# Optimization experiments

Hardware: AMD Instinct MI355X
Metric: run time of the kernel (lower is better)

Reference implementation:

```python
import jax, jax.numpy as jnp
import numpy as np

B, C_HIGH, C_LOW, H, W = 4, 256, 128, 64, 64
HEADS = 4
HEAD_DIM = C_LOW // HEADS
FFN = 2 * C_LOW
EPS = 1e-5


def group_norm1(x, w, b):
    # GroupNorm(num_groups=1): normalize over (C,H,W) per sample, per-channel affine
    mu = jnp.mean(x, axis=(1, 2, 3), keepdims=True)
    var = jnp.var(x, axis=(1, 2, 3), keepdims=True)
    xn = (x - mu) * jax.lax.rsqrt(var + EPS)
    return xn * w[None, :, None, None] + b[None, :, None, None]


def conv1x1(x, Wm):
    # 1x1 conv, no bias: Wm [C_out, C_in], x [B,C_in,H,W]
    return jnp.einsum('oc,bchw->bohw', Wm, x)


def setup_inputs() -> dict:
    key = jax.random.key(0)
    ks = jax.random.split(key, 10)
    s = 0.05
    return {
        'high_feature': jax.random.normal(ks[0], (B, C_HIGH, H, W), jnp.float32),
        'low_feature': jax.random.normal(ks[1], (B, C_LOW, H, W), jnp.float32),
        'norm_high_w': jnp.ones((C_HIGH,), jnp.float32),
        'norm_high_b': jnp.zeros((C_HIGH,), jnp.float32),
        'norm_low_w': jnp.ones((C_LOW,), jnp.float32),
        'norm_low_b': jnp.zeros((C_LOW,), jnp.float32),
        'norm_ffn_w': jnp.ones((C_LOW,), jnp.float32),
        'norm_ffn_b': jnp.zeros((C_LOW,), jnp.float32),
        'Wq': jax.random.normal(ks[2], (C_LOW, C_HIGH), jnp.float32) * s,
        'Wk': jax.random.normal(ks[3], (C_LOW, C_LOW), jnp.float32) * s,
        'Wv': jax.random.normal(ks[4], (C_LOW, C_LOW), jnp.float32) * s,
        'Wproj': jax.random.normal(ks[5], (C_LOW, C_LOW), jnp.float32) * s,
        'Wffn1': jax.random.normal(ks[6], (FFN, C_LOW), jnp.float32) * s,
        'Wffn2': jax.random.normal(ks[7], (C_LOW, FFN), jnp.float32) * s,
        # nn.Parameter(torch.zeros(1)) in the original; use 0.1 for nontrivial grads
        'gamma_attn': jnp.full((1,), 0.1, jnp.float32),
        'gamma_ffn': jnp.full((1,), 0.1, jnp.float32),
    }


def reference(high_feature, low_feature, norm_high_w, norm_high_b, norm_low_w,
              norm_low_b, norm_ffn_w, norm_ffn_b, Wq, Wk, Wv, Wproj, Wffn1,
              Wffn2, gamma_attn, gamma_ffn):
    Bb, _, Hh, Ww = low_feature.shape
    N = Hh * Ww
    scale = HEAD_DIM ** (-0.5)

    high_norm = group_norm1(high_feature, norm_high_w, norm_high_b)
    low_norm = group_norm1(low_feature, norm_low_w, norm_low_b)

    q = conv1x1(high_norm, Wq).reshape(Bb, HEADS, HEAD_DIM, N).transpose(0, 1, 3, 2)  # [B,h,N,d]
    k = conv1x1(low_norm, Wk).reshape(Bb, HEADS, HEAD_DIM, N)                         # [B,h,d,N]
    v = conv1x1(low_norm, Wv).reshape(Bb, HEADS, HEAD_DIM, N).transpose(0, 1, 3, 2)   # [B,h,N,d]

    attn = jax.nn.softmax(jnp.einsum('bhnd,bhdm->bhnm', q, k) * scale, axis=-1)       # [B,h,N,N]
    out = jnp.einsum('bhnm,bhmd->bhnd', attn, v)                                      # [B,h,N,d]
    out = out.transpose(0, 1, 3, 2).reshape(Bb, C_LOW, Hh, Ww)
    out = conv1x1(out, Wproj)

    x = low_feature + gamma_attn[0] * out
    xn = group_norm1(x, norm_ffn_w, norm_ffn_b)
    ffn = conv1x1(jax.nn.gelu(conv1x1(xn, Wffn1), approximate=False), Wffn2)
    return x + gamma_ffn[0] * ffn
```

## Files before the change

### kernel.cpp

```cpp
#include <hip/hip_runtime.h>
#include <hip/hip_bf16.h>
#include <math.h>

#define EPS 1e-5f
#define BB 4
#define CHIGH 256
#define CLOW 128
#define NN 4096
#define NHEADS 4
#define HDIM 32
#define FFN_DIM 256
#define SPLITS 4

typedef __bf16 b8 __attribute__((ext_vector_type(8)));
typedef float f4 __attribute__((ext_vector_type(4)));

__device__ __forceinline__ unsigned int cvt_pk(float lo, float hi) {
    float2 t; t.x = lo; t.y = hi;
    __hip_bfloat162 h = __float22bfloat162_rn(t);
    unsigned int r;
    __builtin_memcpy(&r, &h, sizeof(r));
    return r;
}
__device__ __forceinline__ float b2f(unsigned short u) {
    unsigned int x = ((unsigned int)u) << 16;
    float f;
    __builtin_memcpy(&f, &x, 4);
    return f;
}
__device__ __forceinline__ float fexp2(float x) {
#if __has_builtin(__builtin_amdgcn_exp2f)
    return __builtin_amdgcn_exp2f(x);
#else
    return exp2f(x);
#endif
}

__global__ __launch_bounds__(256)
void prep_kernel(const float* __restrict__ high, const float* __restrict__ low,
                 float* __restrict__ acc,
                 const float* __restrict__ w0, const float* __restrict__ w1,
                 const float* __restrict__ w2, const float* __restrict__ w3,
                 const float* __restrict__ w4, const float* __restrict__ w5,
                 unsigned short* __restrict__ dst)
{
    const int z = blockIdx.z;
    if (z < 2) {
        const int perSample = z == 0 ? CHIGH * NN : CLOW * NN;
        const float* X = z == 0 ? high : low;
        float* ac = acc + (z == 0 ? 0 : 8);
        const int b = blockIdx.y;
        const float4* xp = (const float4*)(X + (size_t)b * perSample);
        const int n4 = perSample >> 2;
        const int stride = gridDim.x * blockDim.x;
        int i = blockIdx.x * blockDim.x + threadIdx.x;
        float s = 0.f, s2 = 0.f, sB = 0.f, s2B = 0.f;
        for (; i + stride < n4; i += 2 * stride) {
            float4 v = xp[i];
            float4 u = xp[i + stride];
            s  += v.x + v.y + v.z + v.w;
            s2 += v.x * v.x + v.y * v.y + v.z * v.z + v.w * v.w;
            sB  += u.x + u.y + u.z + u.w;
            s2B += u.x * u.x + u.y * u.y + u.z * u.z + u.w * u.w;
        }
        if (i < n4) {
            float4 v = xp[i];
            s  += v.x + v.y + v.z + v.w;
            s2 += v.x * v.x + v.y * v.y + v.z * v.z + v.w * v.w;
        }
        s += sB; s2 += s2B;
        for (int off = 32; off; off >>= 1) {
            s  += __shfl_down(s, off, 64);
            s2 += __shfl_down(s2, off, 64);
        }
        __shared__ float ls[4], ls2[4];
        const int w = threadIdx.x >> 6;
        if ((threadIdx.x & 63) == 0) { ls[w] = s; ls2[w] = s2; }
        __syncthreads();
        if (threadIdx.x == 0) {
            atomicAdd(&ac[2 * b], ls[0] + ls[1] + ls[2] + ls[3]);
            atomicAdd(&ac[2 * b + 1], ls2[0] + ls2[1] + ls2[2] + ls2[3]);
        }
    } else {
        const int idx = blockIdx.y * 64 + blockIdx.x;
        const int m = idx >> 5;
        if (m >= 6) return;
        const int sizes[6] = {32768, 16384, 16384, 16384, 32768, 32768};
        const int offs[6]  = {0, 32768, 49152, 65536, 81920, 114688};
        const int Ks[6]    = {256, 128, 128, 128, 128, 256};
        const float* src = m == 0 ? w0 : m == 1 ? w1 : m == 2 ? w2 : m == 3 ? w3
                         : m == 4 ? w4 : w5;
        const int i = ((idx & 31) * 256 + threadIdx.x) * 4;
        if (i >= sizes[m]) return;
        const int K = Ks[m];
        const int row = i / K, col = i % K;
        const int mt = row >> 4, mr = row & 15;
        const int kt = col >> 5, kr = col & 31;
        float4 v = *(const float4*)&src[i];
        uint2 pk;
        pk.x = cvt_pk(v.x, v.y);
        pk.y = cvt_pk(v.z, v.w);
        const int doff = offs[m] + (((mt * (K >> 5)) + kt) << 9) + (mr << 5) + kr;
        *(uint2*)&dst[doff] = pk;
    }
}

__global__ __launch_bounds__(256)
void qkv_kernel(const unsigned short* __restrict__ wbf,
                const float* __restrict__ high, const float* __restrict__ low,
                unsigned short* __restrict__ Qt, unsigned short* __restrict__ Kt,
                unsigned short* __restrict__ Vt,
                const float* __restrict__ nh_w, const float* __restrict__ nh_b,
                const float* __restrict__ nl_w, const float* __restrict__ nl_b,
                const float* __restrict__ st)
{
    __shared__ unsigned short XsRaw[32 * 264];
    const int b = blockIdx.y;
    const int n0 = blockIdx.x * 32;
    const int t = threadIdx.x;
    const int w = t >> 6, lm = t & 15, quad = (t & 63) >> 4;
    const int fo = lm * 32 + quad * 8;
    unsigned int* xw = (unsigned int*)XsRaw;

    if (blockIdx.z == 0) {
        const float invCnt = 1.0f / ((float)CHIGH * NN);
        const float mean = st[2 * b] * invCnt;
        const float rstd = rsqrtf(st[2 * b + 1] * invCnt - mean * mean + EPS);
        const float* Xb = high + (size_t)b * CHIGH * NN;
        float4 ra[4], rb[4];
        float wa[4], wb_[4], ca[4], cb[4];
        #pragma unroll
        for (int it = 0; it < 4; it++) {
            const int s = it * 256 + t;
            const int kp = s >> 3;
            const int k2 = kp << 1;
            const int nc = (s & 7) << 2;
            const size_t ro = (size_t)k2 * NN + n0 + nc;
            ra[it] = *(const float4*)&Xb[ro];
            rb[it] = *(const float4*)&Xb[ro + NN];
            wa[it] = nh_w[k2]; wb_[it] = nh_w[k2 + 1];
            ca[it] = nh_b[k2]; cb[it] = nh_b[k2 + 1];
        }
        #pragma unroll
        for (int it = 0; it < 4; it++) {
            const int s = it * 256 + t;
            const int kp = s >> 3;
            const int nc = (s & 7) << 2;
            float4 pa = ra[it], pb = rb[it];
            const float sc0 = wa[it] * rstd,  sb0 = ca[it] - mean * sc0;
            const float sc1 = wb_[it] * rstd, sb1 = cb[it] - mean * sc1;
            pa.x = pa.x * sc0 + sb0; pa.y = pa.y * sc0 + sb0;
            pa.z = pa.z * sc0 + sb0; pa.w = pa.w * sc0 + sb0;
            pb.x = pb.x * sc1 + sb1; pb.y = pb.y * sc1 + sb1;
            pb.z = pb.z * sc1 + sb1; pb.w = pb.w * sc1 + sb1;
            xw[(nc + 0) * 132 + kp] = cvt_pk(pa.x, pb.x);
            xw[(nc + 1) * 132 + kp] = cvt_pk(pa.y, pb.y);
            xw[(nc + 2) * 132 + kp] = cvt_pk(pa.z, pb.z);
            xw[(nc + 3) * 132 + kp] = cvt_pk(pa.w, pb.w);
        }
        __syncthreads();
        const int ng = w & 1, mh = w >> 1;
        f4 acc[4];
        #pragma unroll
        for (int f = 0; f < 4; f++) acc[f] = (f4){0.f, 0.f, 0.f, 0.f};
        #pragma unroll
        for (int kc = 0; kc < 8; kc++) {
            b8 bx = *(const b8*)&XsRaw[(ng * 16 + lm) * 264 + kc * 32 + quad * 8];
            #pragma unroll
            for (int f = 0; f < 4; f++) {
                b8 af = *(const b8*)&wbf[(((mh * 4 + f) * 8 + kc) << 9) + fo];
                acc[f] = __builtin_amdgcn_mfma_f32_16x16x32_bf16(af, bx, acc[f], 0, 0, 0);
            }
        }
        const int n = n0 + ng * 16 + lm;
        const float oscale = 0.25503480f;
        #pragma unroll
        for (int f = 0; f < 4; f++) {
            const int mb = mh * 64 + f * 16 + quad * 4;
            const int hh = mb >> 5, ddb = mb & 31;
            uint2 pk;
            pk.x = cvt_pk(acc[f][0] * oscale, acc[f][1] * oscale);
            pk.y = cvt_pk(acc[f][2] * oscale, acc[f][3] * oscale);
            *(uint2*)&Qt[((size_t)(b * NHEADS + hh) * NN + n) * 32 + ddb] = pk;
        }
    } else {
        const unsigned short* Wb = wbf + 32768;
        const float invCnt = 1.0f / ((float)CLOW * NN);
        const float mean = st[8 + 2 * b] * invCnt;
        const float rstd = rsqrtf(st[8 + 2 * b + 1] * invCnt - mean * mean + EPS);
        const float* Xb = low + (size_t)b * CLOW * NN;
        float4 ra[2], rb[2];
        float wa[2], wb_[2], ca[2], cb[2];
        #pragma unroll
        for (int it = 0; it < 2; it++) {
            const int s = it * 256 + t;
            const int kp = s >> 3;
            const int k2 = kp << 1;
            const int nc = (s & 7) << 2;
            const size_t ro = (size_t)k2 * NN + n0 + nc;
            ra[it] = *(const float4*)&Xb[ro];
            rb[it] = *(const float4*)&Xb[ro + NN];
            wa[it] = nl_w[k2]; wb_[it] = nl_w[k2 + 1];
            ca[it] = nl_b[k2]; cb[it] = nl_b[k2 + 1];
        }
        #pragma unroll
        for (int it = 0; it < 2; it++) {
            const int s = it * 256 + t;
            const int kp = s >> 3;
            const int nc = (s & 7) << 2;
            float4 pa = ra[it], pb = rb[it];
            const float sc0 = wa[it] * rstd,  sb0 = ca[it] - mean * sc0;
            const float sc1 = wb_[it] * rstd, sb1 = cb[it] - mean * sc1;
            pa.x = pa.x * sc0 + sb0; pa.y = pa.y * sc0 + sb0;
            pa.z = pa.z * sc0 + sb0; pa.w = pa.w * sc0 + sb0;
            pb.x = pb.x * sc1 + sb1; pb.y = pb.y * sc1 + sb1;
            pb.z = pb.z * sc1 + sb1; pb.w = pb.w * sc1 + sb1;
            xw[(nc + 0) * 68 + kp] = cvt_pk(pa.x, pb.x);
            xw[(nc + 1) * 68 + kp] = cvt_pk(pa.y, pb.y);
            xw[(nc + 2) * 68 + kp] = cvt_pk(pa.z, pb.z);
            xw[(nc + 3) * 68 + kp] = cvt_pk(pa.w, pb.w);
        }
        __syncthreads();
        f4 acc[2][4];
        #pragma unroll
        for (int ng = 0; ng < 2; ng++)
            #pragma unroll
            for (int f = 0; f < 4; f++) acc[ng][f] = (f4){0.f, 0.f, 0.f, 0.f};
        #pragma unroll
        for (int kc = 0; kc < 4; kc++) {
            b8 bx0 = *(const b8*)&XsRaw[lm * 136 + kc * 32 + quad * 8];
            b8 bx1 = *(const b8*)&XsRaw[(16 + lm) * 136 + kc * 32 + quad * 8];
            #pragma unroll
            for (int f = 0; f < 4; f++) {
                b8 af = *(const b8*)&Wb[(((w * 4 + f) * 4 + kc) << 9) + fo];
                acc[0][f] = __builtin_amdgcn_mfma_f32_16x16x32_bf16(af, bx0, acc[0][f], 0, 0, 0);
                acc[1][f] = __builtin_amdgcn_mfma_f32_16x16x32_bf16(af, bx1, acc[1][f], 0, 0, 0);
            }
        }
        if (w < 2) {
            #pragma unroll
            for (int ng = 0; ng < 2; ng++) {
                const int n = n0 + ng * 16 + lm;
                #pragma unroll
                for (int f = 0; f < 4; f++) {
                    const int mb = w * 64 + f * 16 + quad * 4;
                    const int hh = mb >> 5, ddb = mb & 31;
                    uint2 pk;
                    pk.x = cvt_pk(acc[ng][f][0], acc[ng][f][1]);
                    pk.y = cvt_pk(acc[ng][f][2], acc[ng][f][3]);
                    *(uint2*)&Kt[((size_t)(b * NHEADS + hh) * NN + n) * 32 + ddb] = pk;
                }
            }
        } else {
            #pragma unroll
            for (int ng = 0; ng < 2; ng++) {
                const int n = n0 + ng * 16 + lm;
                const size_t nblk = ((size_t)(n >> 5) << 10) + (n & 31);
                #pragma unroll
                for (int f = 0; f < 4; f++) {
                    const int db = (w - 2) * 64 + f * 16 + quad * 4;
                    const int hh = db >> 5;
                    const size_t hb = (size_t)(b * NHEADS + hh) * NN * 32;
                    #pragma unroll
                    for (int r = 0; r < 4; r++) {
                        const int d = (db + r) & 31;
                        unsigned int u = cvt_pk(acc[ng][f][r], 0.f);
                        Vt[hb + nblk + (size_t)d * 32] = (unsigned short)(u & 0xFFFF);
                    }
                }
            }
        }
    }
}

__global__ __launch_bounds__(512)
void flash_kernel(const unsigned short* __restrict__ Qt,
                  const unsigned short* __restrict__ Kt,
                  const unsigned short* __restrict__ Vt,
                  unsigned short* __restrict__ Op, float* __restrict__ Lp)
{
    __shared__ unsigned short Ps[8][32][72];

    const int lid = blockIdx.x;
    const int xcd = lid & 7, slot = lid >> 3;
    const int g = xcd * 8 + (slot >> 4);
    const int xblk = slot & 15;
    const int half = g >> 4, bh = g & 15;
    const int b = bh >> 2, h = bh & 3;
    const int n0 = xblk * 256;
    const int t = threadIdx.x;
    const int w = t >> 6;
    const int lm = t & 15, quad = (t & 63) >> 4;

    const unsigned short* Qh = Qt + (size_t)(b * NHEADS + h) * NN * 32;
    const unsigned short* Kh = Kt + (size_t)(b * NHEADS + h) * NN * 32;
    const unsigned short* Vh = Vt + (size_t)(b * NHEADS + h) * NN * 32;

    b8 aq[2];
    aq[0] = *(const b8*)&Qh[(size_t)(n0 + w * 32 + lm) * 32 + quad * 8];
    aq[1] = *(const b8*)&Qh[(size_t)(n0 + w * 32 + 16 + lm) * 32 + quad * 8];

    b8 ones;
    #pragma unroll
    for (int j = 0; j < 8; j++) ones[j] = (__bf16)1.0f;

    f4 ocT[2][2];
    f4 lsum[2];
    #pragma unroll
    for (int u = 0; u < 2; u++) {
        lsum[u] = (f4){0.f, 0.f, 0.f, 0.f};
        ocT[0][u] = (f4){0.f, 0.f, 0.f, 0.f};
        ocT[1][u] = (f4){0.f, 0.f, 0.f, 0.f};
    }

    const int m_lo = half * (NN / SPLITS), m_hi = m_lo + NN / SPLITS;
    for (int m0 = m_lo; m0 < m_hi; m0 += 64) {
        b8 bk[4], av[2][2];
        #pragma unroll
        for (int f = 0; f < 4; f++)
            bk[f] = *(const b8*)&Kh[(size_t)(m0 + f * 16 + lm) * 32 + quad * 8];
        #pragma unroll
        for (int c = 0; c < 2; c++) {
            const size_t vb = (size_t)(m0 + c * 32) * 32 + quad * 8;
            av[0][c] = *(const b8*)&Vh[vb + (size_t)lm * 32];
            av[1][c] = *(const b8*)&Vh[vb + (size_t)(16 + lm) * 32];
        }

        f4 st[4][2];
        #pragma unroll
        for (int f = 0; f < 4; f++)
            #pragma unroll
            for (int u = 0; u < 2; u++) {
                f4 z = {0.f, 0.f, 0.f, 0.f};
                st[f][u] = __builtin_amdgcn_mfma_f32_16x16x32_bf16(bk[f], aq[u], z, 0, 0, 0);
            }

        #pragma unroll
        for (int f = 0; f < 4; f++)
            #pragma unroll
            for (int u = 0; u < 2; u++) {
                uint2 pk;
                pk.x = cvt_pk(fexp2(st[f][u][0]), fexp2(st[f][u][1]));
                pk.y = cvt_pk(fexp2(st[f][u][2]), fexp2(st[f][u][3]));
                *(uint2*)&Ps[w][u * 16 + lm][f * 16 + quad * 4] = pk;
            }

        #pragma unroll
        for (int c = 0; c < 2; c++)
            #pragma unroll
            for (int u = 0; u < 2; u++) {
                b8 bp = *(const b8*)&Ps[w][u * 16 + lm][c * 32 + quad * 8];
                ocT[0][u] = __builtin_amdgcn_mfma_f32_16x16x32_bf16(av[0][c], bp, ocT[0][u], 0, 0, 0);
                ocT[1][u] = __builtin_amdgcn_mfma_f32_16x16x32_bf16(av[1][c], bp, ocT[1][u], 0, 0, 0);
                lsum[u]   = __builtin_amdgcn_mfma_f32_16x16x32_bf16(ones, bp, lsum[u], 0, 0, 0);
            }
    }

    unsigned short* OpB = Op + ((size_t)(half * BB + b) * CLOW + h * HDIM) * NN;
    float* LpB = Lp + ((size_t)(half * BB + b) * NHEADS + h) * NN;
    #pragma unroll
    for (int u = 0; u < 2; u++) {
        const int n = n0 + w * 32 + u * 16 + lm;
        if (quad == 0) LpB[n] = lsum[u][0];
        #pragma unroll
        for (int hh = 0; hh < 2; hh++)
            #pragma unroll
            for (int r = 0; r < 4; r++) {
                const int d = hh * 16 + quad * 4 + r;
                unsigned int uu = cvt_pk(ocT[hh][u][r], 0.f);
                OpB[(size_t)d * NN + n] = (unsigned short)(uu & 0xFFFF);
            }
    }
}

__global__ __launch_bounds__(256)
void proj_kernel(const unsigned short* __restrict__ Wb,
                 const unsigned short* __restrict__ Opart, const float* __restrict__ Lp,
                 const float* __restrict__ low, float* __restrict__ Xout,
                 const float* __restrict__ gp, float* __restrict__ stOut)
{
    __shared__ unsigned short Xs[32][136];
    __shared__ float red[8];
    const int b = blockIdx.y;
    const int n0 = blockIdx.x * 32;
    const int t = threadIdx.x;
    const int w = t >> 6, lm = t & 15, quad = (t & 63) >> 4;
    const int fo = lm * 32 + quad * 8;
    unsigned int* xw = (unsigned int*)&Xs[0][0];

    #pragma unroll
    for (int it = 0; it < 2; it++) {
        const int s = it * 256 + t;
        const int kp = s >> 3;
        const int k2 = kp << 1;
        const int nc = (s & 7) << 2;
        const size_t ro = (size_t)k2 * NN + n0 + nc;
        const int hh = k2 >> 5;
        const size_t lo = (size_t)(b * NHEADS + hh) * NN + n0 + nc;
        float4 l4 = *(const float4*)&Lp[lo];
        #pragma unroll
        for (int sp = 1; sp < SPLITS; sp++)
            l4 += *(const float4*)&Lp[lo + (size_t)sp * BB * NHEADS * NN];
        float4 pa = {0.f, 0.f, 0.f, 0.f}, pb = {0.f, 0.f, 0.f, 0.f};
        #pragma unroll
        for (int sp = 0; sp < SPLITS; sp++) {
            const unsigned short* Os = Opart + (size_t)sp * BB * CLOW * NN
                                     + (size_t)b * CLOW * NN + ro;
            ushort4 ua = *(const ushort4*)Os;
            ushort4 ub = *(const ushort4*)(Os + NN);
            pa.x += b2f(ua.x); pa.y += b2f(ua.y); pa.z += b2f(ua.z); pa.w += b2f(ua.w);
            pb.x += b2f(ub.x); pb.y += b2f(ub.y); pb.z += b2f(ub.z); pb.w += b2f(ub.w);
        }
        float4 iv;
        iv.x = 1.f / l4.x; iv.y = 1.f / l4.y; iv.z = 1.f / l4.z; iv.w = 1.f / l4.w;
        pa.x *= iv.x; pa.y *= iv.y; pa.z *= iv.z; pa.w *= iv.w;
        pb.x *= iv.x; pb.y *= iv.y; pb.z *= iv.z; pb.w *= iv.w;
        xw[(nc + 0) * 68 + kp] = cvt_pk(pa.x, pb.x);
        xw[(nc + 1) * 68 + kp] = cvt_pk(pa.y, pb.y);
        xw[(nc + 2) * 68 + kp] = cvt_pk(pa.z, pb.z);
        xw[(nc + 3) * 68 + kp] = cvt_pk(pa.w, pb.w);
    }
    __syncthreads();

    f4 acc[2][2];
    #pragma unroll
    for (int f = 0; f < 2; f++) {
        acc[f][0] = (f4){0.f, 0.f, 0.f, 0.f};
        acc[f][1] = (f4){0.f, 0.f, 0.f, 0.f};
    }
    #pragma unroll
    for (int kc = 0; kc < 4; kc++) {
        b8 bx0 = *(const b8*)&Xs[lm][kc * 32 + quad * 8];
        b8 bx1 = *(const b8*)&Xs[16 + lm][kc * 32 + quad * 8];
        #pragma unroll
        for (int f = 0; f < 2; f++) {
            const int mt = w * 2 + f;
            b8 af = *(const b8*)&Wb[((mt * 4 + kc) << 9) + fo];
            acc[f][0] = __builtin_amdgcn_mfma_f32_16x16x32_bf16(af, bx0, acc[f][0], 0, 0, 0);
            acc[f][1] = __builtin_amdgcn_mfma_f32_16x16x32_bf16(af, bx1, acc[f][1], 0, 0, 0);
        }
    }

    const float g = gp[0];
    const float* Rb = low + (size_t)b * CLOW * NN;
    float* Yb = Xout + (size_t)b * CLOW * NN;
    float s = 0.f, s2 = 0.f;
    #pragma unroll
    for (int f = 0; f < 2; f++)
        #pragma unroll
        for (int ng = 0; ng < 2; ng++) {
            const int n = n0 + ng * 16 + lm;
            #pragma unroll
            for (int r = 0; r < 4; r++) {
                const int m = w * 32 + f * 16 + quad * 4 + r;
                const size_t off = (size_t)m * NN + n;
                float v = Rb[off] + g * acc[f][ng][r];
                Yb[off] = v;
                s += v; s2 += v * v;
            }
        }
    for (int off = 32; off; off >>= 1) {
        s  += __shfl_down(s, off, 64);
        s2 += __shfl_down(s2, off, 64);
    }
    if ((t & 63) == 0) { red[w] = s; red[4 + w] = s2; }
    __syncthreads();
    if (t == 0) {
        atomicAdd(&stOut[2 * b], red[0] + red[1] + red[2] + red[3]);
        atomicAdd(&stOut[2 * b + 1], red[4] + red[5] + red[6] + red[7]);
    }
}

__global__ __launch_bounds__(512)
void ffn_kernel(const unsigned short* __restrict__ W1, const unsigned short* __restrict__ W2,
                const float* __restrict__ X, float* __restrict__ Out,
                const float* __restrict__ nw, const float* __restrict__ nb,
                const float* __restrict__ st, const float* __restrict__ gp)
{
    __shared__ unsigned short Xs[32][136];
    __shared__ unsigned short Hs[32][264];
    const int b = blockIdx.y;
    const int n0 = blockIdx.x * 32;
    const int t = threadIdx.x;
    const int w = t >> 6, lm = t & 15, quad = (t & 63) >> 4;
    const int fo = lm * 32 + quad * 8;

    const float invCnt = 1.0f / ((float)CLOW * NN);
    const float mean = st[2 * b] * invCnt;
    const float rstd = rsqrtf(st[2 * b + 1] * invCnt - mean * mean + EPS);

    const float* Xb = X + (size_t)b * CLOW * NN;
    unsigned int* xw = (unsigned int*)&Xs[0][0];
    {
        const int s = t;
        const int kp = s >> 3;
        const int k2 = kp << 1;
        const int nc = (s & 7) << 2;
        const size_t ro = (size_t)k2 * NN + n0 + nc;
        float4 pa = *(const float4*)&Xb[ro];
        float4 pb = *(const float4*)&Xb[ro + NN];
        const float sc0 = nw[k2] * rstd,     sb0 = nb[k2] - mean * sc0;
        const float sc1 = nw[k2 + 1] * rstd, sb1 = nb[k2 + 1] - mean * sc1;
        pa.x = pa.x * sc0 + sb0; pa.y = pa.y * sc0 + sb0;
        pa.z = pa.z * sc0 + sb0; pa.w = pa.w * sc0 + sb0;
        pb.x = pb.x * sc1 + sb1; pb.y = pb.y * sc1 + sb1;
        pb.z = pb.z * sc1 + sb1; pb.w = pb.w * sc1 + sb1;
        xw[(nc + 0) * 68 + kp] = cvt_pk(pa.x, pb.x);
        xw[(nc + 1) * 68 + kp] = cvt_pk(pa.y, pb.y);
        xw[(nc + 2) * 68 + kp] = cvt_pk(pa.z, pb.z);
        xw[(nc + 3) * 68 + kp] = cvt_pk(pa.w, pb.w);
    }
    __syncthreads();

    f4 hv[2][2];
    #pragma unroll
    for (int ng = 0; ng < 2; ng++) {
        hv[ng][0] = (f4){0.f, 0.f, 0.f, 0.f};
        hv[ng][1] = (f4){0.f, 0.f, 0.f, 0.f};
    }
    #pragma unroll
    for (int kc = 0; kc < 4; kc++) {
        b8 bx0 = *(const b8*)&Xs[lm][kc * 32 + quad * 8];
        b8 bx1 = *(const b8*)&Xs[16 + lm][kc * 32 + quad * 8];
        #pragma unroll
        for (int f = 0; f < 2; f++) {
            const int mt = w * 2 + f;
            b8 af = *(const b8*)&W1[((mt * 4 + kc) << 9) + fo];
            hv[0][f] = __builtin_amdgcn_mfma_f32_16x16x32_bf16(af, bx0, hv[0][f], 0, 0, 0);
            hv[1][f] = __builtin_amdgcn_mfma_f32_16x16x32_bf16(af, bx1, hv[1][f], 0, 0, 0);
        }
    }
    #pragma unroll
    for (int ng = 0; ng < 2; ng++)
        #pragma unroll
        for (int f = 0; f < 2; f++) {
            float g0 = hv[ng][f][0], g1 = hv[ng][f][1];
            float g2 = hv[ng][f][2], g3 = hv[ng][f][3];
            g0 = 0.5f * g0 * (1.f + erff(g0 * 0.70710678118654752f));
            g1 = 0.5f * g1 * (1.f + erff(g1 * 0.70710678118654752f));
            g2 = 0.5f * g2 * (1.f + erff(g2 * 0.70710678118654752f));
            g3 = 0.5f * g3 * (1.f + erff(g3 * 0.70710678118654752f));
            uint2 pk;
            pk.x = cvt_pk(g0, g1);
            pk.y = cvt_pk(g2, g3);
            *(uint2*)&Hs[ng * 16 + lm][w * 32 + f * 16 + quad * 4] = pk;
        }
    __syncthreads();

    f4 o[2];
    o[0] = (f4){0.f, 0.f, 0.f, 0.f};
    o[1] = (f4){0.f, 0.f, 0.f, 0.f};
    #pragma unroll
    for (int kc = 0; kc < 8; kc++) {
        b8 bh0 = *(const b8*)&Hs[lm][kc * 32 + quad * 8];
        b8 bh1 = *(const b8*)&Hs[16 + lm][kc * 32 + quad * 8];
        b8 af = *(const b8*)&W2[((w * 8 + kc) << 9) + fo];
        o[0] = __builtin_amdgcn_mfma_f32_16x16x32_bf16(af, bh0, o[0], 0, 0, 0);
        o[1] = __builtin_amdgcn_mfma_f32_16x16x32_bf16(af, bh1, o[1], 0, 0, 0);
    }
    const float g = gp[0];
    float* Ob = Out + (size_t)b * CLOW * NN;
    #pragma unroll
    for (int ng = 0; ng < 2; ng++) {
        const int n = n0 + ng * 16 + lm;
        #pragma unroll
        for (int r = 0; r < 4; r++) {
            const int m = w * 16 + quad * 4 + r;
            const size_t off = (size_t)m * NN + n;
            Ob[off] = Xb[off] + g * o[ng][r];
        }
    }
}

extern "C" void kernel_launch(void* const* d_in, const int* in_sizes, int n_in,
                              void* d_out, int out_size, void* d_ws, size_t ws_size,
                              hipStream_t stream)
{
    const float* high  = (const float*)d_in[0];
    const float* low   = (const float*)d_in[1];
    const float* nh_w  = (const float*)d_in[2];
    const float* nh_b  = (const float*)d_in[3];
    const float* nl_w  = (const float*)d_in[4];
    const float* nl_b  = (const float*)d_in[5];
    const float* nf_w  = (const float*)d_in[6];
    const float* nf_b  = (const float*)d_in[7];
    const float* Wq    = (const float*)d_in[8];
    const float* Wk    = (const float*)d_in[9];
    const float* Wv    = (const float*)d_in[10];
    const float* Wproj = (const float*)d_in[11];
    const float* Wff1  = (const float*)d_in[12];
    const float* Wff2  = (const float*)d_in[13];
    const float* g_at  = (const float*)d_in[14];
    const float* g_ff  = (const float*)d_in[15];
    float* out = (float*)d_out;

    float* ws    = (float*)d_ws;
    float* stats = ws;
    unsigned short* wbf = (unsigned short*)(ws + 64);
    unsigned short* qt = wbf + 147456;
    unsigned short* kt = qt + (size_t)BB * NHEADS * NN * 32;
    unsigned short* vt = kt + (size_t)BB * NHEADS * NN * 32;
    unsigned short* opart = vt + (size_t)BB * CLOW * NN;
    float* lpart = (float*)(opart + (size_t)SPLITS * BB * CLOW * NN);
    float* x     = lpart + (size_t)SPLITS * BB * NHEADS * NN;

    (void)hipMemsetAsync(stats, 0, 64 * sizeof(float), stream);

    prep_kernel<<<dim3(64, BB, 3), 256, 0, stream>>>(high, low, stats,
                                                     Wq, Wk, Wv, Wproj, Wff1, Wff2, wbf);

    qkv_kernel<<<dim3(128, BB, 2), 256, 0, stream>>>(wbf, high, low, qt, kt, vt,
                                                     nh_w, nh_b, nl_w, nl_b, stats);

    flash_kernel<<<dim3(1024), 512, 0, stream>>>(qt, kt, vt, opart, lpart);

    proj_kernel<<<dim3(128, BB), 256, 0, stream>>>(wbf + 65536, opart, lpart,
                                                   low, x, g_at, stats + 16);

    ffn_kernel<<<dim3(128, BB), 512, 0, stream>>>(wbf + 81920, wbf + 114688, x, out,
                                                  nf_w, nf_b, stats + 16, g_ff);
}
```

Measured before the change: 220.1 us.

## Store residual x in bf16, halve proj tile width, shrink LDS padding

The intermediate residual x written by proj_kernel and read by ffn_kernel is now stored as bf16 rather than fp32, which halves that round trip through global memory. proj_kernel now handles 16 columns per block with twice as many blocks to expose more parallelism. The LDS row strides in several kernels drop from +8 to +4 bf16 padding, which changes the bank-conflict pattern. The final residual add now uses a bf16-rounded x, which loses precision in the output, while the norm statistics are still accumulated from the fp32 values.

```diff
diff --git a/kernel.cpp b/kernel.cpp
--- a/kernel.cpp
+++ b/kernel.cpp
@@ -21,6 +21,10 @@
     unsigned int r;
     __builtin_memcpy(&r, &h, sizeof(r));
     return r;
+}
+__device__ __forceinline__ unsigned short f2bs(float v) {
+    unsigned int u = cvt_pk(v, 0.f);
+    return (unsigned short)(u & 0xFFFF);
 }
 __device__ __forceinline__ float b2f(unsigned short u) {
     unsigned int x = ((unsigned int)u) << 16;
@@ -114,7 +118,7 @@
                 const float* __restrict__ nl_w, const float* __restrict__ nl_b,
                 const float* __restrict__ st)
 {
-    __shared__ unsigned short XsRaw[32 * 264];
+    __shared__ unsigned short XsRaw[32 * 260];
     const int b = blockIdx.y;
     const int n0 = blockIdx.x * 32;
     const int t = threadIdx.x;
@@ -153,10 +157,10 @@
             pa.z = pa.z * sc0 + sb0; pa.w = pa.w * sc0 + sb0;
             pb.x = pb.x * sc1 + sb1; pb.y = pb.y * sc1 + sb1;
             pb.z = pb.z * sc1 + sb1; pb.w = pb.w * sc1 + sb1;
-            xw[(nc + 0) * 132 + kp] = cvt_pk(pa.x, pb.x);
-            xw[(nc + 1) * 132 + kp] = cvt_pk(pa.y, pb.y);
-            xw[(nc + 2) * 132 + kp] = cvt_pk(pa.z, pb.z);
-            xw[(nc + 3) * 132 + kp] = cvt_pk(pa.w, pb.w);
+            xw[(nc + 0) * 130 + kp] = cvt_pk(pa.x, pb.x);
+            xw[(nc + 1) * 130 + kp] = cvt_pk(pa.y, pb.y);
+            xw[(nc + 2) * 130 + kp] = cvt_pk(pa.z, pb.z);
+            xw[(nc + 3) * 130 + kp] = cvt_pk(pa.w, pb.w);
         }
         __syncthreads();
         const int ng = w & 1, mh = w >> 1;
@@ -165,7 +169,7 @@
         for (int f = 0; f < 4; f++) acc[f] = (f4){0.f, 0.f, 0.f, 0.f};
         #pragma unroll
         for (int kc = 0; kc < 8; kc++) {
-            b8 bx = *(const b8*)&XsRaw[(ng * 16 + lm) * 264 + kc * 32 + quad * 8];
+            b8 bx = *(const b8*)&XsRaw[(ng * 16 + lm) * 260 + kc * 32 + quad * 8];
             #pragma unroll
             for (int f = 0; f < 4; f++) {
                 b8 af = *(const b8*)&wbf[(((mh * 4 + f) * 8 + kc) << 9) + fo];
@@ -215,10 +219,10 @@
             pa.z = pa.z * sc0 + sb0; pa.w = pa.w * sc0 + sb0;
             pb.x = pb.x * sc1 + sb1; pb.y = pb.y * sc1 + sb1;
             pb.z = pb.z * sc1 + sb1; pb.w = pb.w * sc1 + sb1;
-            xw[(nc + 0) * 68 + kp] = cvt_pk(pa.x, pb.x);
-            xw[(nc + 1) * 68 + kp] = cvt_pk(pa.y, pb.y);
-            xw[(nc + 2) * 68 + kp] = cvt_pk(pa.z, pb.z);
-            xw[(nc + 3) * 68 + kp] = cvt_pk(pa.w, pb.w);
+            xw[(nc + 0) * 66 + kp] = cvt_pk(pa.x, pb.x);
+            xw[(nc + 1) * 66 + kp] = cvt_pk(pa.y, pb.y);
+            xw[(nc + 2) * 66 + kp] = cvt_pk(pa.z, pb.z);
+            xw[(nc + 3) * 66 + kp] = cvt_pk(pa.w, pb.w);
         }
         __syncthreads();
         f4 acc[2][4];
@@ -228,8 +232,8 @@
             for (int f = 0; f < 4; f++) acc[ng][f] = (f4){0.f, 0.f, 0.f, 0.f};
         #pragma unroll
         for (int kc = 0; kc < 4; kc++) {
-            b8 bx0 = *(const b8*)&XsRaw[lm * 136 + kc * 32 + quad * 8];
-            b8 bx1 = *(const b8*)&XsRaw[(16 + lm) * 136 + kc * 32 + quad * 8];
+            b8 bx0 = *(const b8*)&XsRaw[lm * 132 + kc * 32 + quad * 8];
+            b8 bx1 = *(const b8*)&XsRaw[(16 + lm) * 132 + kc * 32 + quad * 8];
             #pragma unroll
             for (int f = 0; f < 4; f++) {
                 b8 af = *(const b8*)&Wb[(((w * 4 + f) * 4 + kc) << 9) + fo];
@@ -264,8 +268,7 @@
                     #pragma unroll
                     for (int r = 0; r < 4; r++) {
                         const int d = (db + r) & 31;
-                        unsigned int u = cvt_pk(acc[ng][f][r], 0.f);
-                        Vt[hb + nblk + (size_t)d * 32] = (unsigned short)(u & 0xFFFF);
+                        Vt[hb + nblk + (size_t)d * 32] = f2bs(acc[ng][f][r]);
                     }
                 }
             }
@@ -367,8 +370,7 @@
             #pragma unroll
             for (int r = 0; r < 4; r++) {
                 const int d = hh * 16 + quad * 4 + r;
-                unsigned int uu = cvt_pk(ocT[hh][u][r], 0.f);
-                OpB[(size_t)d * NN + n] = (unsigned short)(uu & 0xFFFF);
+                OpB[(size_t)d * NN + n] = f2bs(ocT[hh][u][r]);
             }
     }
 }
@@ -376,24 +378,22 @@
 __global__ __launch_bounds__(256)
 void proj_kernel(const unsigned short* __restrict__ Wb,
                  const unsigned short* __restrict__ Opart, const float* __restrict__ Lp,
-                 const float* __restrict__ low, float* __restrict__ Xout,
+                 const float* __restrict__ low, unsigned short* __restrict__ Xout,
                  const float* __restrict__ gp, float* __restrict__ stOut)
 {
-    __shared__ unsigned short Xs[32][136];
+    __shared__ unsigned short Xs[16 * 132];
     __shared__ float red[8];
     const int b = blockIdx.y;
-    const int n0 = blockIdx.x * 32;
+    const int n0 = blockIdx.x * 16;
     const int t = threadIdx.x;
     const int w = t >> 6, lm = t & 15, quad = (t & 63) >> 4;
     const int fo = lm * 32 + quad * 8;
-    unsigned int* xw = (unsigned int*)&Xs[0][0];
-
-    #pragma unroll
-    for (int it = 0; it < 2; it++) {
-        const int s = it * 256 + t;
-        const int kp = s >> 3;
+    unsigned int* xw = (unsigned int*)Xs;
+
+    {
+        const int kp = t >> 2;
         const int k2 = kp << 1;
-        const int nc = (s & 7) << 2;
+        const int nc = (t & 3) << 2;
         const size_t ro = (size_t)k2 * NN + n0 + nc;
         const int hh = k2 >> 5;
         const size_t lo = (size_t)(b * NHEADS + hh) * NN + n0 + nc;
@@ -415,49 +415,41 @@
         iv.x = 1.f / l4.x; iv.y = 1.f / l4.y; iv.z = 1.f / l4.z; iv.w = 1.f / l4.w;
         pa.x *= iv.x; pa.y *= iv.y; pa.z *= iv.z; pa.w *= iv.w;
         pb.x *= iv.x; pb.y *= iv.y; pb.z *= iv.z; pb.w *= iv.w;
-        xw[(nc + 0) * 68 + kp] = cvt_pk(pa.x, pb.x);
-        xw[(nc + 1) * 68 + kp] = cvt_pk(pa.y, pb.y);
-        xw[(nc + 2) * 68 + kp] = cvt_pk(pa.z, pb.z);
-        xw[(nc + 3) * 68 + kp] = cvt_pk(pa.w, pb.w);
+        xw[(nc + 0) * 66 + kp] = cvt_pk(pa.x, pb.x);
+        xw[(nc + 1) * 66 + kp] = cvt_pk(pa.y, pb.y);
+        xw[(nc + 2) * 66 + kp] = cvt_pk(pa.z, pb.z);
+        xw[(nc + 3) * 66 + kp] = cvt_pk(pa.w, pb.w);
     }
     __syncthreads();
 
-    f4 acc[2][2];
-    #pragma unroll
-    for (int f = 0; f < 2; f++) {
-        acc[f][0] = (f4){0.f, 0.f, 0.f, 0.f};
-        acc[f][1] = (f4){0.f, 0.f, 0.f, 0.f};
-    }
+    f4 acc[2];
+    acc[0] = (f4){0.f, 0.f, 0.f, 0.f};
+    acc[1] = (f4){0.f, 0.f, 0.f, 0.f};
     #pragma unroll
     for (int kc = 0; kc < 4; kc++) {
-        b8 bx0 = *(const b8*)&Xs[lm][kc * 32 + quad * 8];
-        b8 bx1 = *(const b8*)&Xs[16 + lm][kc * 32 + quad * 8];
+        b8 bx = *(const b8*)&Xs[lm * 132 + kc * 32 + quad * 8];
         #pragma unroll
         for (int f = 0; f < 2; f++) {
             const int mt = w * 2 + f;
             b8 af = *(const b8*)&Wb[((mt * 4 + kc) << 9) + fo];
-            acc[f][0] = __builtin_amdgcn_mfma_f32_16x16x32_bf16(af, bx0, acc[f][0], 0, 0, 0);
-            acc[f][1] = __builtin_amdgcn_mfma_f32_16x16x32_bf16(af, bx1, acc[f][1], 0, 0, 0);
+            acc[f] = __builtin_amdgcn_mfma_f32_16x16x32_bf16(af, bx, acc[f], 0, 0, 0);
         }
     }
 
     const float g = gp[0];
     const float* Rb = low + (size_t)b * CLOW * NN;
-    float* Yb = Xout + (size_t)b * CLOW * NN;
+    unsigned short* Yb = Xout + (size_t)b * CLOW * NN;
+    const int n = n0 + lm;
     float s = 0.f, s2 = 0.f;
     #pragma unroll
     for (int f = 0; f < 2; f++)
         #pragma unroll
-        for (int ng = 0; ng < 2; ng++) {
-            const int n = n0 + ng * 16 + lm;
-            #pragma unroll
-            for (int r = 0; r < 4; r++) {
-                const int m = w * 32 + f * 16 + quad * 4 + r;
-                const size_t off = (size_t)m * NN + n;
-                float v = Rb[off] + g * acc[f][ng][r];
-                Yb[off] = v;
-                s += v; s2 += v * v;
-            }
+        for (int r = 0; r < 4; r++) {
+            const int m = w * 32 + f * 16 + quad * 4 + r;
+            const size_t off = (size_t)m * NN + n;
+            float v = Rb[off] + g * acc[f][r];
+            Yb[off] = f2bs(v);
+            s += v; s2 += v * v;
         }
     for (int off = 32; off; off >>= 1) {
         s  += __shfl_down(s, off, 64);
@@ -473,11 +465,11 @@
 
 __global__ __launch_bounds__(512)
 void ffn_kernel(const unsigned short* __restrict__ W1, const unsigned short* __restrict__ W2,
-                const float* __restrict__ X, float* __restrict__ Out,
+                const unsigned short* __restrict__ X, float* __restrict__ Out,
                 const float* __restrict__ nw, const float* __restrict__ nb,
                 const float* __restrict__ st, const float* __restrict__ gp)
 {
-    __shared__ unsigned short Xs[32][136];
+    __shared__ unsigned short Xs[32 * 132];
     __shared__ unsigned short Hs[32][264];
     const int b = blockIdx.y;
     const int n0 = blockIdx.x * 32;
@@ -489,26 +481,28 @@
     const float mean = st[2 * b] * invCnt;
     const float rstd = rsqrtf(st[2 * b + 1] * invCnt - mean * mean + EPS);
 
-    const float* Xb = X + (size_t)b * CLOW * NN;
-    unsigned int* xw = (unsigned int*)&Xs[0][0];
+    const unsigned short* Xb = X + (size_t)b * CLOW * NN;
+    unsigned int* xw = (unsigned int*)Xs;
     {
-        const int s = t;
-        const int kp = s >> 3;
+        const int kp = t >> 3;
         const int k2 = kp << 1;
-        const int nc = (s & 7) << 2;
+        const int nc = (t & 7) << 2;
         const size_t ro = (size_t)k2 * NN + n0 + nc;
-        float4 pa = *(const float4*)&Xb[ro];
-        float4 pb = *(const float4*)&Xb[ro + NN];
+        ushort4 ua = *(const ushort4*)&Xb[ro];
+        ushort4 ub = *(const ushort4*)&Xb[ro + NN];
+        float4 pa, pb;
+        pa.x = b2f(ua.x); pa.y = b2f(ua.y); pa.z = b2f(ua.z); pa.w = b2f(ua.w);
+        pb.x = b2f(ub.x); pb.y = b2f(ub.y); pb.z = b2f(ub.z); pb.w = b2f(ub.w);
         const float sc0 = nw[k2] * rstd,     sb0 = nb[k2] - mean * sc0;
         const float sc1 = nw[k2 + 1] * rstd, sb1 = nb[k2 + 1] - mean * sc1;
         pa.x = pa.x * sc0 + sb0; pa.y = pa.y * sc0 + sb0;
         pa.z = pa.z * sc0 + sb0; pa.w = pa.w * sc0 + sb0;
         pb.x = pb.x * sc1 + sb1; pb.y = pb.y * sc1 + sb1;
         pb.z = pb.z * sc1 + sb1; pb.w = pb.w * sc1 + sb1;
-        xw[(nc + 0) * 68 + kp] = cvt_pk(pa.x, pb.x);
-        xw[(nc + 1) * 68 + kp] = cvt_pk(pa.y, pb.y);
-        xw[(nc + 2) * 68 + kp] = cvt_pk(pa.z, pb.z);
-        xw[(nc + 3) * 68 + kp] = cvt_pk(pa.w, pb.w);
+        xw[(nc + 0) * 66 + kp] = cvt_pk(pa.x, pb.x);
+        xw[(nc + 1) * 66 + kp] = cvt_pk(pa.y, pb.y);
+        xw[(nc + 2) * 66 + kp] = cvt_pk(pa.z, pb.z);
+        xw[(nc + 3) * 66 + kp] = cvt_pk(pa.w, pb.w);
     }
     __syncthreads();
 
@@ -520,8 +514,8 @@
     }
     #pragma unroll
     for (int kc = 0; kc < 4; kc++) {
-        b8 bx0 = *(const b8*)&Xs[lm][kc * 32 + quad * 8];
-        b8 bx1 = *(const b8*)&Xs[16 + lm][kc * 32 + quad * 8];
+        b8 bx0 = *(const b8*)&Xs[lm * 132 + kc * 32 + quad * 8];
+        b8 bx1 = *(const b8*)&Xs[(16 + lm) * 132 + kc * 32 + quad * 8];
         #pragma unroll
         for (int f = 0; f < 2; f++) {
             const int mt = w * 2 + f;
@@ -567,7 +561,7 @@
         for (int r = 0; r < 4; r++) {
             const int m = w * 16 + quad * 4 + r;
             const size_t off = (size_t)m * NN + n;
-            Ob[off] = Xb[off] + g * o[ng][r];
+            Ob[off] = b2f(Xb[off]) + g * o[ng][r];
         }
     }
 }
@@ -602,7 +596,7 @@
     unsigned short* vt = kt + (size_t)BB * NHEADS * NN * 32;
     unsigned short* opart = vt + (size_t)BB * CLOW * NN;
     float* lpart = (float*)(opart + (size_t)SPLITS * BB * CLOW * NN);
-    float* x     = lpart + (size_t)SPLITS * BB * NHEADS * NN;
+    unsigned short* xbf = (unsigned short*)(lpart + (size_t)SPLITS * BB * NHEADS * NN);
 
     (void)hipMemsetAsync(stats, 0, 64 * sizeof(float), stream);
 
@@ -614,9 +608,9 @@
 
     flash_kernel<<<dim3(1024), 512, 0, stream>>>(qt, kt, vt, opart, lpart);
 
-    proj_kernel<<<dim3(128, BB), 256, 0, stream>>>(wbf + 65536, opart, lpart,
-                                                   low, x, g_at, stats + 16);
-
-    ffn_kernel<<<dim3(128, BB), 512, 0, stream>>>(wbf + 81920, wbf + 114688, x, out,
+    proj_kernel<<<dim3(256, BB), 256, 0, stream>>>(wbf + 65536, opart, lpart,
+                                                   low, xbf, g_at, stats + 16);
+
+    ffn_kernel<<<dim3(128, BB), 512, 0, stream>>>(wbf + 81920, wbf + 114688, xbf, out,
                                                   nf_w, nf_b, stats + 16, g_ff);
 }
```

After: 233.8 us. 6.2% more time.
